# Optimization experiments

Measured on AMD Instinct MI355X. Metric: run time of the kernel, lower is better.

## Reference

```python
import jax, jax.numpy as jnp
import numpy as np

CRIT = 15          # critical_dimension
GAMMA = 0.2        # gamma_param
DELTA = 0.03       # delta_param
THETA_NC = 1e-35   # theta_noncomm
MAXD = 100         # max_dimension


def _build_theta(dim):
    i = jnp.arange(dim)
    # theta[i,j] = theta_nc * (-1)^(i+j) for j>i, antisymmetric, zero diag
    sign = jnp.where(((i[:, None] + i[None, :]) % 2) == 0, 1.0, -1.0)
    antisym = jnp.sign(i[None, :] - i[:, None]).astype(jnp.float32)
    return (THETA_NC * sign * antisym).astype(jnp.float32)


def setup_inputs() -> dict:
    key = jax.random.key(0)
    k1, k2 = jax.random.split(key)
    B, IN = 4096, 100
    x = jax.random.uniform(k1, (B, IN), dtype=jnp.float32)
    W = jax.random.normal(k2, (MAXD, MAXD), dtype=jnp.float32)
    theta = _build_theta(MAXD)
    return {"x": x, "inner_coefficients": W, "theta_matrix": theta, "dimension": 100}


def _forward(x, W, theta, dimension):
    B, IN = x.shape
    D = int(dimension)
    P = min(IN, D)

    # ---- inner functions phi_{q,p}(x_p), vectorized over (q, p) ----
    q = jnp.arange(D, dtype=jnp.float32)
    k = q + 1.0
    # superconvergence factor S_q (only used for q >= CRIT; where() guards q<CRIT)
    S = 1.0 + GAMMA * jnp.log(q / CRIT) * (1.0 - jnp.exp(-DELTA * (q - CRIT)))
    coeff = jnp.where(q < CRIT, 1.0 / k, 1.0 / (k * S))          # [D]
    exp_term = jnp.exp(-DELTA * k * k)                            # [D]
    sin_term = jnp.sin(jnp.pi * k[None, :, None] * x[:, None, :P])  # [B,D,P]
    inner_p = (coeff * exp_term)[None, :, None] * sin_term * W[:D, :P][None]
    inner = jnp.pad(inner_p, ((0, 0), (0, 0), (0, IN - P)))      # [B,D,IN], zero pad like torch

    # ---- outer functions: Chebyshev recurrence on mean(tanh(sum_p inner)) ----
    x_norm = jnp.tanh(inner.sum(-1))          # [B,D]
    x_mean = jnp.mean(x_norm, axis=-1)        # [B]
    N = 2 * D + 1
    T0 = jnp.ones_like(x_mean)
    T1 = x_mean

    def cheb_step(carry, _):
        tm2, tm1 = carry
        tn = 2.0 * x_mean * tm1 - tm2
        return (tm1, tn), tn

    _, rest = jax.lax.scan(cheb_step, (T0, T1), None, length=N - 2)  # [N-2, B]
    outer = jnp.concatenate([T0[:, None], T1[:, None], rest.T], axis=1)  # [B, 2D+1]

    # ---- noncommutative composition (Moyal-Weyl star product) ----
    inner_mean = inner.mean(-1)                 # [B,D]
    product = outer[:, :D] * inner_mean         # [B,D]
    R = min(D, theta.shape[0], IN)
    th = theta[:R, :R]
    # sum_{mu!=nu} (inner_mu - inner_nu) * theta[mu,nu]  (diag(theta)=0)
    grad_sum = jnp.einsum('bqm,m->bq', inner[:, :, :R], th.sum(1) - th.sum(0))
    # correction = Re(0.5j * grad_sum); grad_sum is real, so the real part is 0
    corr = 0.0 * grad_sum
    return product + corr


def reference(x, inner_coefficients, theta_matrix, dimension):
    return _forward(x, inner_coefficients, theta_matrix, dimension)
```

## Files before the change

kernel.cpp:

```cpp
#include <hip/hip_runtime.h>
#include <math.h>


#define IN_DIM 100
#define MAXD   100
#define NP4    (IN_DIM / 4)
#define WAVES  8
#define BLK    (WAVES * 64)
#define RPW    2
#define ROWS   (WAVES * RPW)
#define INV2PI 0.15915494309189535f

__device__ __forceinline__ float fast_tanh(float v) {
    float e = __expf(2.0f * v);
    return 1.0f - 2.0f / (e + 1.0f);
}

__global__ __launch_bounds__(BLK) void kat_kernel(
    const float* __restrict__ x, const float* __restrict__ W,
    const int* __restrict__ dimp, float* __restrict__ out, int B)
{
    const int D = *dimp;
    const int P = (IN_DIM < D) ? IN_DIM : D;

    __shared__ float4 cw4[NP4][MAXD];

    const int t = threadIdx.x;

    for (int idx = t; idx < NP4 * MAXD; idx += BLK) {
        int p4 = idx / MAXD;
        int q  = idx - p4 * MAXD;
        float k = (float)(q + 1);
        float c;
        if (q < 15) {
            c = 1.0f / k;
        } else {
            float qf = (float)q;
            float S = 1.0f + 0.2f * __logf(qf / 15.0f) * (1.0f - __expf(-0.03f * (qf - 15.0f)));
            c = 1.0f / (k * S);
        }
        c = (q < D) ? c * __expf(-0.03f * k * k) : 0.0f;
        float4 wv = ((const float4*)W)[q * (MAXD / 4) + p4];
        int p = 4 * p4;
        float4 v;
        v.x = (p     < P) ? c * wv.x : 0.0f;
        v.y = (p + 1 < P) ? c * wv.y : 0.0f;
        v.z = (p + 2 < P) ? c * wv.z : 0.0f;
        v.w = (p + 3 < P) ? c * wv.w : 0.0f;
        cw4[p4][q] = v;
    }
    __syncthreads();

    const int w    = t >> 6;
    const int lane = t & 63;
    const int row0 = blockIdx.x * ROWS;
    const int bA   = row0 + w * RPW;
    const int bB   = bA + 1;

    int buA = __builtin_amdgcn_readfirstlane((bA < B) ? bA : (B - 1));
    int buB = __builtin_amdgcn_readfirstlane((bB < B) ? bB : (B - 1));
    const float4* __restrict__ xA4 = (const float4*)(x + (size_t)buA * IN_DIM);
    const float4* __restrict__ xB4 = (const float4*)(x + (size_t)buB * IN_DIM);

    const int q0  = lane;
    const int q1  = lane + 64;
    const int q1c = (q1 < MAXD - 1) ? q1 : (MAXD - 1);
    const float m1 = (q1 < D) ? 1.0f : 0.0f;

    const float f0 = 0.5f * (float)(q0 + 1);
    const float f1 = 0.5f * (float)(q1 + 1);

    float a0A = 0.0f, a1A = 0.0f, a0B = 0.0f, a1B = 0.0f;
    #pragma unroll 5
    for (int p4 = 0; p4 < NP4; ++p4) {
        float4 xa = xA4[p4];
        float4 xb = xB4[p4];
        float4 c0 = cw4[p4][q0];
        float4 c1 = cw4[p4][q1c];

        a0A = fmaf(__builtin_amdgcn_sinf(f0 * xa.x), c0.x, a0A);
        a1A = fmaf(__builtin_amdgcn_sinf(f1 * xa.x), c1.x, a1A);
        a0B = fmaf(__builtin_amdgcn_sinf(f0 * xb.x), c0.x, a0B);
        a1B = fmaf(__builtin_amdgcn_sinf(f1 * xb.x), c1.x, a1B);

        a0A = fmaf(__builtin_amdgcn_sinf(f0 * xa.y), c0.y, a0A);
        a1A = fmaf(__builtin_amdgcn_sinf(f1 * xa.y), c1.y, a1A);
        a0B = fmaf(__builtin_amdgcn_sinf(f0 * xb.y), c0.y, a0B);
        a1B = fmaf(__builtin_amdgcn_sinf(f1 * xb.y), c1.y, a1B);

        a0A = fmaf(__builtin_amdgcn_sinf(f0 * xa.z), c0.z, a0A);
        a1A = fmaf(__builtin_amdgcn_sinf(f1 * xa.z), c1.z, a1A);
        a0B = fmaf(__builtin_amdgcn_sinf(f0 * xb.z), c0.z, a0B);
        a1B = fmaf(__builtin_amdgcn_sinf(f1 * xb.z), c1.z, a1B);

        a0A = fmaf(__builtin_amdgcn_sinf(f0 * xa.w), c0.w, a0A);
        a1A = fmaf(__builtin_amdgcn_sinf(f1 * xa.w), c1.w, a1A);
        a0B = fmaf(__builtin_amdgcn_sinf(f0 * xb.w), c0.w, a0B);
        a1B = fmaf(__builtin_amdgcn_sinf(f1 * xb.w), c1.w, a1B);
    }
    a1A *= m1;
    a1B *= m1;

    float sA = fast_tanh(a0A) + fast_tanh(a1A);
    float sB = fast_tanh(a0B) + fast_tanh(a1B);
    #pragma unroll
    for (int m = 32; m; m >>= 1) {
        sA += __shfl_xor(sA, m);
        sB += __shfl_xor(sB, m);
    }
    const float thA = acosf(sA / (float)D) * INV2PI;
    const float thB = acosf(sB / (float)D) * INV2PI;
    const float inv = 1.0f / (float)IN_DIM;

    if (bA < B) {
        if (q0 < D) out[bA * D + q0] = __builtin_amdgcn_cosf((float)q0 * thA) * a0A * inv;
        if (q1 < D) out[bA * D + q1] = __builtin_amdgcn_cosf((float)q1 * thA) * a1A * inv;
    }
    if (bB < B) {
        if (q0 < D) out[bB * D + q0] = __builtin_amdgcn_cosf((float)q0 * thB) * a0B * inv;
        if (q1 < D) out[bB * D + q1] = __builtin_amdgcn_cosf((float)q1 * thB) * a1B * inv;
    }
}

extern "C" void kernel_launch(void* const* d_in, const int* in_sizes, int n_in,
                              void* d_out, int out_size, void* d_ws, size_t ws_size,
                              hipStream_t stream) {
    const float* x    = (const float*)d_in[0];
    const float* W    = (const float*)d_in[1];
    const int*   dimp = (const int*)d_in[3];
    float*       out  = (float*)d_out;

    const int B = in_sizes[0] / IN_DIM;
    const int grid = (B + ROWS - 1) / ROWS;

    hipLaunchKernelGGL(kat_kernel, dim3(grid), dim3(BLK), 0, stream,
                       x, W, dimp, out, B);
}
```

Baseline: 15.99 us.

## Use one row per wave and stage x rows in shared memory

Each wave now processes a single batch row instead of two, which doubles the grid to 512 blocks. The block's x rows are loaded into LDS cooperatively rather than each wave reading them from global memory with scalar loads. This is meant to improve occupancy and CU coverage for a small batch. In exchange, the per-block setup of the cw4 coefficient table (exp/log work and W loads) is repeated across twice as many blocks, and each row's x values are now read through LDS.

After: 16.46 us. 3.0% more time.

```diff
diff --git a/kernel.cpp b/kernel.cpp
--- a/kernel.cpp
+++ b/kernel.cpp
@@ -7,8 +7,7 @@
 #define NP4    (IN_DIM / 4)
 #define WAVES  8
 #define BLK    (WAVES * 64)
-#define RPW    2
-#define ROWS   (WAVES * RPW)
+#define ROWS   WAVES
 #define INV2PI 0.15915494309189535f
 
 __device__ __forceinline__ float fast_tanh(float v) {
@@ -24,9 +23,20 @@
     const int P = (IN_DIM < D) ? IN_DIM : D;
 
     __shared__ float4 cw4[NP4][MAXD];
+    __shared__ float  xr[ROWS][IN_DIM];
 
     const int t = threadIdx.x;
+    const int row0 = blockIdx.x * ROWS;
 
+    {
+        const float4* x4 = (const float4*)(x + (size_t)row0 * IN_DIM);
+        for (int i = t; i < ROWS * NP4; i += BLK) {
+            int r = i / NP4;
+            int p = (i - r * NP4) * 4;
+            float4 v = (row0 + r < B) ? x4[i] : make_float4(0.f, 0.f, 0.f, 0.f);
+            xr[r][p] = v.x; xr[r][p+1] = v.y; xr[r][p+2] = v.z; xr[r][p+3] = v.w;
+        }
+    }
     for (int idx = t; idx < NP4 * MAXD; idx += BLK) {
         int p4 = idx / MAXD;
         int q  = idx - p4 * MAXD;
@@ -53,14 +63,7 @@
 
     const int w    = t >> 6;
     const int lane = t & 63;
-    const int row0 = blockIdx.x * ROWS;
-    const int bA   = row0 + w * RPW;
-    const int bB   = bA + 1;
-
-    int buA = __builtin_amdgcn_readfirstlane((bA < B) ? bA : (B - 1));
-    int buB = __builtin_amdgcn_readfirstlane((bB < B) ? bB : (B - 1));
-    const float4* __restrict__ xA4 = (const float4*)(x + (size_t)buA * IN_DIM);
-    const float4* __restrict__ xB4 = (const float4*)(x + (size_t)buB * IN_DIM);
+    const int b    = row0 + w;
 
     const int q0  = lane;
     const int q1  = lane + 64;
@@ -70,55 +73,35 @@
     const float f0 = 0.5f * (float)(q0 + 1);
     const float f1 = 0.5f * (float)(q1 + 1);
 
-    float a0A = 0.0f, a1A = 0.0f, a0B = 0.0f, a1B = 0.0f;
+    const float4* __restrict__ xw4 = (const float4*)&xr[w][0];
+
+    float a0 = 0.0f, a1 = 0.0f;
     #pragma unroll 5
     for (int p4 = 0; p4 < NP4; ++p4) {
-        float4 xa = xA4[p4];
-        float4 xb = xB4[p4];
+        float4 xv = xw4[p4];
         float4 c0 = cw4[p4][q0];
         float4 c1 = cw4[p4][q1c];
 
-        a0A = fmaf(__builtin_amdgcn_sinf(f0 * xa.x), c0.x, a0A);
-        a1A = fmaf(__builtin_amdgcn_sinf(f1 * xa.x), c1.x, a1A);
-        a0B = fmaf(__builtin_amdgcn_sinf(f0 * xb.x), c0.x, a0B);
-        a1B = fmaf(__builtin_amdgcn_sinf(f1 * xb.x), c1.x, a1B);
+        a0 = fmaf(__builtin_amdgcn_sinf(f0 * xv.x), c0.x, a0);
+        a1 = fmaf(__builtin_amdgcn_sinf(f1 * xv.x), c1.x, a1);
+        a0 = fmaf(__builtin_amdgcn_sinf(f0 * xv.y), c0.y, a0);
+        a1 = fmaf(__builtin_amdgcn_sinf(f1 * xv.y), c1.y, a1);
+        a0 = fmaf(__builtin_amdgcn_sinf(f0 * xv.z), c0.z, a0);
+        a1 = fmaf(__builtin_amdgcn_sinf(f1 * xv.z), c1.z, a1);
+        a0 = fmaf(__builtin_amdgcn_sinf(f0 * xv.w), c0.w, a0);
+        a1 = fmaf(__builtin_amdgcn_sinf(f1 * xv.w), c1.w, a1);
+    }
+    a1 *= m1;
 
-        a0A = fmaf(__builtin_amdgcn_sinf(f0 * xa.y), c0.y, a0A);
-        a1A = fmaf(__builtin_amdgcn_sinf(f1 * xa.y), c1.y, a1A);
-        a0B = fmaf(__builtin_amdgcn_sinf(f0 * xb.y), c0.y, a0B);
-        a1B = fmaf(__builtin_amdgcn_sinf(f1 * xb.y), c1.y, a1B);
+    float s = fast_tanh(a0) + fast_tanh(a1);
+    #pragma unroll
+    for (int m = 32; m; m >>= 1) s += __shfl_xor(s, m);
 
-        a0A = fmaf(__builtin_amdgcn_sinf(f0 * xa.z), c0.z, a0A);
-        a1A = fmaf(__builtin_amdgcn_sinf(f1 * xa.z), c1.z, a1A);
-        a0B = fmaf(__builtin_amdgcn_sinf(f0 * xb.z), c0.z, a0B);
-        a1B = fmaf(__builtin_amdgcn_sinf(f1 * xb.z), c1.z, a1B);
-
-        a0A = fmaf(__builtin_amdgcn_sinf(f0 * xa.w), c0.w, a0A);
-        a1A = fmaf(__builtin_amdgcn_sinf(f1 * xa.w), c1.w, a1A);
-        a0B = fmaf(__builtin_amdgcn_sinf(f0 * xb.w), c0.w, a0B);
-        a1B = fmaf(__builtin_amdgcn_sinf(f1 * xb.w), c1.w, a1B);
-    }
-    a1A *= m1;
-    a1B *= m1;
-
-    float sA = fast_tanh(a0A) + fast_tanh(a1A);
-    float sB = fast_tanh(a0B) + fast_tanh(a1B);
-    #pragma unroll
-    for (int m = 32; m; m >>= 1) {
-        sA += __shfl_xor(sA, m);
-        sB += __shfl_xor(sB, m);
-    }
-    const float thA = acosf(sA / (float)D) * INV2PI;
-    const float thB = acosf(sB / (float)D) * INV2PI;
+    const float thr = acosf(s / (float)D) * INV2PI;
     const float inv = 1.0f / (float)IN_DIM;
-
-    if (bA < B) {
-        if (q0 < D) out[bA * D + q0] = __builtin_amdgcn_cosf((float)q0 * thA) * a0A * inv;
-        if (q1 < D) out[bA * D + q1] = __builtin_amdgcn_cosf((float)q1 * thA) * a1A * inv;
-    }
-    if (bB < B) {
-        if (q0 < D) out[bB * D + q0] = __builtin_amdgcn_cosf((float)q0 * thB) * a0B * inv;
-        if (q1 < D) out[bB * D + q1] = __builtin_amdgcn_cosf((float)q1 * thB) * a1B * inv;
+    if (b < B) {
+        if (q0 < D) out[b * D + q0] = __builtin_amdgcn_cosf((float)q0 * thr) * a0 * inv;
+        if (q1 < D) out[b * D + q1] = __builtin_amdgcn_cosf((float)q1 * thr) * a1 * inv;
     }
 }
 
```
